# Optimization experiments

Hardware: AMD Instinct MI355X
Metric: run time of the kernel (lower is better)

Reference implementation:

```python
import jax, jax.numpy as jnp
import numpy as np

N, C, H, W = 16, 256, 128, 128
TC = max(8, C // 32)  # temp_c
EPS = 1e-5


def setup_inputs() -> dict:
    key = jax.random.key(0)
    ks = jax.random.split(key, 10)
    x = jax.random.normal(ks[0], (N, C, H, W), jnp.float32)
    # conv1: 1x1, C -> TC (weight squeezed to [TC, C])
    w1 = jax.random.normal(ks[1], (TC, C), jnp.float32) * 0.05
    b1 = jnp.zeros((TC,), jnp.float32)
    # BatchNorm2d (inference form)
    bn_gamma = jnp.ones((TC,), jnp.float32)
    bn_beta = jnp.zeros((TC,), jnp.float32)
    bn_mean = jnp.zeros((TC,), jnp.float32)
    bn_var = jnp.ones((TC,), jnp.float32)
    # conv2: kernel (1,2), TC -> C, squeezed to [C, TC, 2]
    w2 = jax.random.normal(ks[2], (C, TC, 2), jnp.float32) * 0.1
    b2 = jnp.zeros((C,), jnp.float32)
    # conv3: kernel (2,1), TC -> C, squeezed to [C, TC, 2]
    w3 = jax.random.normal(ks[3], (C, TC, 2), jnp.float32) * 0.1
    b3 = jnp.zeros((C,), jnp.float32)
    # conv4: kernel (1,2), TC -> C, squeezed to [C, TC, 2]
    w4 = jax.random.normal(ks[4], (C, TC, 2), jnp.float32) * 0.1
    b4 = jnp.zeros((C,), jnp.float32)
    return dict(x=x, w1=w1, b1=b1, bn_gamma=bn_gamma, bn_beta=bn_beta,
                bn_mean=bn_mean, bn_var=bn_var, w2=w2, b2=b2, w3=w3, b3=b3,
                w4=w4, b4=b4)


def reference(x, w1, b1, bn_gamma, bn_beta, bn_mean, bn_var,
              w2, b2, w3, b3, w4, b4):
    n, c, Hh, Ww = x.shape
    # avg/max pools along W (per-row), H (per-col), and global (per-channel)
    cat_h = jnp.stack([x.mean(3), x.max(3)], axis=-1)            # [n,c,H,2]
    cat_w = jnp.stack([x.mean(2), x.max(2)], axis=-1)            # [n,c,W,2]
    cat_c = jnp.stack([x.mean((2, 3)), x.max((2, 3))], -1)[:, :, None, :]  # [n,c,1,2]
    x_cat = jnp.concatenate([cat_h, cat_w, cat_c], axis=2)       # [n,c,H+W+1,2]
    # 1x1 conv + BN (inference) + h_swish
    y = jnp.einsum('ncsk,tc->ntsk', x_cat, w1) + b1[None, :, None, None]
    inv = bn_gamma / jnp.sqrt(bn_var + EPS)
    y = (y - bn_mean[None, :, None, None]) * inv[None, :, None, None] \
        + bn_beta[None, :, None, None]
    y = y * jnp.clip(y + 3.0, 0.0, 6.0) / 6.0                    # h_swish
    # split
    xh = y[:, :, :Hh, :]               # [n,tc,H,2]
    xw = y[:, :, Hh:Hh + Ww, :]        # [n,tc,W,2]
    xc = y[:, :, Hh + Ww, :]           # [n,tc,2]
    # tiny convs (kernels collapse to contractions over (tc, k)) + sigmoid
    a_h = jax.nn.sigmoid(jnp.einsum('nthk,otk->noh', xh, w2) + b2[None, :, None])  # [n,C,H]
    a_w = jax.nn.sigmoid(jnp.einsum('ntwk,otk->now', xw, w3) + b3[None, :, None])  # [n,C,W]
    a_c = jax.nn.sigmoid(jnp.einsum('ntk,otk->no', xc, w4) + b4[None, :])          # [n,C]
    return x * a_w[:, :, None, :] * a_h[:, :, :, None] * a_c[:, :, None, None]
```

## Files before the change

kernel.cpp:

```cpp
#include <hip/hip_runtime.h>
#include <math.h>

#define N_ 16
#define C_ 256
#define H_ 128
#define W_ 128
#define TC_ 8
#define S_ 257
#define EPS_ 1e-5f
#define NBLK 512
#define BPN 32
#define PPB 8

#define XCT_OFF  0
#define AH_OFF   2105344
#define AW_OFF   (AH_OFF + 524288)
#define Y256_OFF (AW_OFF + 524288)

typedef float f4n __attribute__((ext_vector_type(4)));

__global__ __launch_bounds__(256, 2) void k1_stats(
    const float* __restrict__ x, float* __restrict__ xcat)
{
    const int b = blockIdx.x;
    const int tid = threadIdx.x;
    __shared__ __align__(16) float smf[9472];

    float2 (*rowp)[33] = reinterpret_cast<float2(*)[33]>(smf);
    float4* scr_s = reinterpret_cast<float4*>(smf + 8448);
    float4* scr_m = reinterpret_cast<float4*>(smf + 8960);
    const int rg = tid >> 5;

    for (int u = 0; u < PPB; ++u) {
        const int p = b * PPB + u;
        const float4* xt = reinterpret_cast<const float4*>(x) + (size_t)p * 4096;
        float2* xcat2 = reinterpret_cast<float2*>(xcat) + (size_t)p * S_;

        float4 cs = make_float4(0.f, 0.f, 0.f, 0.f);
        float4 cm = make_float4(-INFINITY, -INFINITY, -INFINITY, -INFINITY);

        #pragma unroll
        for (int k = 0; k < 16; ++k) {
            const float4 v = xt[k * 256 + tid];
            cs.x += v.x; cs.y += v.y; cs.z += v.z; cs.w += v.w;
            cm.x = fmaxf(cm.x, v.x); cm.y = fmaxf(cm.y, v.y);
            cm.z = fmaxf(cm.z, v.z); cm.w = fmaxf(cm.w, v.w);
            const float rs = (v.x + v.y) + (v.z + v.w);
            const float rm = fmaxf(fmaxf(v.x, v.y), fmaxf(v.z, v.w));
            rowp[k * 8 + rg][tid & 31] = make_float2(rs, rm);
        }

        cs.x += __shfl_xor(cs.x, 32); cs.y += __shfl_xor(cs.y, 32);
        cs.z += __shfl_xor(cs.z, 32); cs.w += __shfl_xor(cs.w, 32);
        cm.x = fmaxf(cm.x, __shfl_xor(cm.x, 32));
        cm.y = fmaxf(cm.y, __shfl_xor(cm.y, 32));
        cm.z = fmaxf(cm.z, __shfl_xor(cm.z, 32));
        cm.w = fmaxf(cm.w, __shfl_xor(cm.w, 32));

        const int wv = tid >> 6, ln = tid & 63;
        if (ln < 32) { scr_s[wv * 32 + ln] = cs; scr_m[wv * 32 + ln] = cm; }
        __syncthreads();

        if (tid >= 128) {
            const int h = tid - 128;
            float2 q0 = rowp[h][0];
            float s = q0.x, m = q0.y;
            #pragma unroll
            for (int j = 1; j < 32; ++j) {
                const float2 q = rowp[h][j];
                s += q.x; m = fmaxf(m, q.y);
            }
            xcat2[h] = make_float2(s * (1.f / 128.f), m);
        }

        if (tid < 32) {
            const float4 s0 = scr_s[tid],      s1 = scr_s[32 + tid],
                         s2 = scr_s[64 + tid], s3 = scr_s[96 + tid];
            const float4 m0 = scr_m[tid],      m1 = scr_m[32 + tid],
                         m2 = scr_m[64 + tid], m3 = scr_m[96 + tid];
            float4 S, M;
            S.x = (s0.x + s1.x) + (s2.x + s3.x);
            S.y = (s0.y + s1.y) + (s2.y + s3.y);
            S.z = (s0.z + s1.z) + (s2.z + s3.z);
            S.w = (s0.w + s1.w) + (s2.w + s3.w);
            M.x = fmaxf(fmaxf(m0.x, m1.x), fmaxf(m2.x, m3.x));
            M.y = fmaxf(fmaxf(m0.y, m1.y), fmaxf(m2.y, m3.y));
            M.z = fmaxf(fmaxf(m0.z, m1.z), fmaxf(m2.z, m3.z));
            M.w = fmaxf(fmaxf(m0.w, m1.w), fmaxf(m2.w, m3.w));

            const int w0 = 4 * tid;
            xcat2[128 + w0 + 0] = make_float2(S.x * (1.f / 128.f), M.x);
            xcat2[128 + w0 + 1] = make_float2(S.y * (1.f / 128.f), M.y);
            xcat2[128 + w0 + 2] = make_float2(S.z * (1.f / 128.f), M.z);
            xcat2[128 + w0 + 3] = make_float2(S.w * (1.f / 128.f), M.w);

            float gs = (S.x + S.y) + (S.z + S.w);
            float gm = fmaxf(fmaxf(M.x, M.y), fmaxf(M.z, M.w));
            #pragma unroll
            for (int m = 16; m >= 1; m >>= 1) {
                gs += __shfl_xor(gs, m);
                gm = fmaxf(gm, __shfl_xor(gm, m));
            }
            if (tid == 0) xcat2[256] = make_float2(gs * (1.f / 16384.f), gm);
        }
        __syncthreads();
    }
}

__global__ __launch_bounds__(256, 2) void k2_attn(
    const float* __restrict__ xcat,
    const float* __restrict__ w1, const float* __restrict__ b1,
    const float* __restrict__ gam, const float* __restrict__ bet,
    const float* __restrict__ mu, const float* __restrict__ var,
    const float* __restrict__ w2, const float* __restrict__ b2,
    const float* __restrict__ w3, const float* __restrict__ b3,
    float* __restrict__ ahg, float* __restrict__ awg, float* __restrict__ y256g)
{
    const int b = blockIdx.x;
    const int n = b >> 5, cg = b & 31;
    const int tid = threadIdx.x;
    __shared__ __align__(16) float smf[6448];

    float* w1s = smf;
    float* red = smf + 2048;
    float* ys  = smf + 6272;
    const float2* xc2 = reinterpret_cast<const float2*>(xcat) + (size_t)n * C_ * S_;
    const int s0 = cg * 8;

    for (int i = tid; i < TC_ * C_; i += 256) w1s[i] = w1[i];
    __syncthreads();

    {
        const int cgrp = tid >> 3, si = tid & 7;
        const int s = s0 + si;
        float acc[16];
        #pragma unroll
        for (int j = 0; j < 16; ++j) acc[j] = 0.f;
        #pragma unroll
        for (int i = 0; i < 8; ++i) {
            const int c = cgrp * 8 + i;
            const float2 v = xc2[c * S_ + s];
            #pragma unroll
            for (int t = 0; t < TC_; ++t) {
                const float w = w1s[t * C_ + c];
                acc[t * 2 + 0] += v.x * w;
                acc[t * 2 + 1] += v.y * w;
            }
        }
        #pragma unroll
        for (int j = 0; j < 16; ++j) red[(si * 16 + j) * 33 + cgrp] = acc[j];
    }
    __syncthreads();

    if (tid < 128) {
        const int si2 = tid >> 4, j = tid & 15, t = j >> 1;
        float z = 0.f;
        #pragma unroll
        for (int g = 0; g < 32; ++g) z += red[(si2 * 16 + j) * 33 + g];
        const float inv = gam[t] * rsqrtf(var[t] + EPS_);
        float y = (z + b1[t] - mu[t]) * inv + bet[t];
        y = y * fminf(fmaxf(y + 3.f, 0.f), 6.f) * (1.f / 6.f);
        ys[si2 * 17 + j] = y;
    }
    __syncthreads();

    if (cg == BPN - 1) {
        const int c = tid;
        const float2 v = xc2[c * S_ + 256];
        float pj[16];
        #pragma unroll
        for (int t = 0; t < TC_; ++t) {
            const float w = w1s[t * C_ + c];
            pj[t * 2 + 0] = v.x * w;
            pj[t * 2 + 1] = v.y * w;
        }
        __syncthreads();
        float* red2 = smf;
        float* redB = smf + 4400;
        #pragma unroll
        for (int j = 0; j < 16; ++j) red2[tid * 17 + j] = pj[j];
        __syncthreads();
        {
            const int g = tid >> 4, j = tid & 15;
            float z = 0.f;
            #pragma unroll
            for (int m = 0; m < 16; ++m) z += red2[(g * 16 + m) * 17 + j];
            redB[j * 17 + g] = z;
        }
        __syncthreads();
        if (tid < 16) {
            const int j = tid, t = j >> 1;
            float z = 0.f;
            #pragma unroll
            for (int g = 0; g < 16; ++g) z += redB[j * 17 + g];
            const float inv = gam[t] * rsqrtf(var[t] + EPS_);
            float y = (z + b1[t] - mu[t]) * inv + bet[t];
            y = y * fminf(fmaxf(y + 3.f, 0.f), 6.f) * (1.f / 6.f);
            y256g[n * 16 + j] = y;
        }
        __syncthreads();
    }

    {
        const int o = tid;
        const bool is_h = (cg < 16);
        const float* wX = is_h ? w2 : w3;
        const float zb = is_h ? b2[o] : b3[o];
        float4 wr[4];
        const float4* wv = reinterpret_cast<const float4*>(wX + o * 16);
        #pragma unroll
        for (int q = 0; q < 4; ++q) wr[q] = wv[q];

        float r[8];
        #pragma unroll
        for (int si = 0; si < 8; ++si) {
            float z = zb;
            #pragma unroll
            for (int q = 0; q < 4; ++q) {
                z += ys[si * 17 + q * 4 + 0] * wr[q].x
                   + ys[si * 17 + q * 4 + 1] * wr[q].y
                   + ys[si * 17 + q * 4 + 2] * wr[q].z
                   + ys[si * 17 + q * 4 + 3] * wr[q].w;
            }
            r[si] = 1.f / (1.f + expf(-z));
        }
        float* og = is_h ? (ahg + (size_t)(n * C_ + o) * H_ + s0)
                         : (awg + (size_t)(n * C_ + o) * W_ + (s0 - 128));
        *reinterpret_cast<float4*>(og)     = make_float4(r[0], r[1], r[2], r[3]);
        *reinterpret_cast<float4*>(og + 4) = make_float4(r[4], r[5], r[6], r[7]);
    }
}

__global__ __launch_bounds__(256, 2) void k3_apply(
    const float* __restrict__ x,
    const float* __restrict__ w4, const float* __restrict__ b4,
    const float* __restrict__ ahg, const float* __restrict__ awg,
    const float* __restrict__ y256g, float* __restrict__ out)
{
    const int b = blockIdx.x;
    const int n = b >> 5, cg = b & 31, c0 = cg * 8;
    const int tid = threadIdx.x;
    __shared__ __align__(16) float smf[2064];

    float* acs = smf;
    float* ahl = smf + 16;
    float* awl = smf + 1040;

    if (tid < 8) {
        const int o = c0 + tid;
        float z = b4[o];
        #pragma unroll
        for (int j = 0; j < 16; ++j) z += y256g[n * 16 + j] * w4[o * 16 + j];
        acs[tid] = 1.f / (1.f + expf(-z));
    }
    __syncthreads();

    for (int idx = tid; idx < 8 * 128; idx += 256) {
        const int u = idx >> 7, h = idx & 127, o = c0 + u;
        ahl[idx] = acs[u] * ahg[(size_t)(n * C_ + o) * H_ + h];
        awl[idx] = awg[(size_t)(n * C_ + o) * W_ + h];
    }
    __syncthreads();

    const float4* awv = reinterpret_cast<const float4*>(awl);
    for (int u = 0; u < PPB; ++u) {
        const int p = b * PPB + u;
        const f4n* x4 = reinterpret_cast<const f4n*>(x) + (size_t)p * 4096;
        f4n* o4 = reinterpret_cast<f4n*>(out) + (size_t)p * 4096;

        const float4 a = awv[u * 32 + (tid & 31)];
        #pragma unroll
        for (int k = 0; k < 16; ++k) {
            const int i4 = k * 256 + tid;
            f4n v = x4[i4];
            const float s = ahl[u * 128 + k * 8 + (tid >> 5)];
            v.x *= s * a.x; v.y *= s * a.y; v.z *= s * a.z; v.w *= s * a.w;
            __builtin_nontemporal_store(v, &o4[i4]);
        }
    }
}

extern "C" void kernel_launch(void* const* d_in, const int* in_sizes, int n_in,
                              void* d_out, int out_size, void* d_ws, size_t ws_size,
                              hipStream_t stream) {
    const float* x   = (const float*)d_in[0];
    const float* w1  = (const float*)d_in[1];
    const float* b1  = (const float*)d_in[2];
    const float* gam = (const float*)d_in[3];
    const float* bet = (const float*)d_in[4];
    const float* mu  = (const float*)d_in[5];
    const float* var = (const float*)d_in[6];
    const float* w2  = (const float*)d_in[7];
    const float* b2  = (const float*)d_in[8];
    const float* w3  = (const float*)d_in[9];
    const float* b3  = (const float*)d_in[10];
    const float* w4  = (const float*)d_in[11];
    const float* b4  = (const float*)d_in[12];

    float* ws    = (float*)d_ws;
    float* xcat  = ws + XCT_OFF;
    float* ahg   = ws + AH_OFF;
    float* awg   = ws + AW_OFF;
    float* y256g = ws + Y256_OFF;
    float* out   = (float*)d_out;

    k1_stats<<<NBLK, 256, 0, stream>>>(x, xcat);
    k2_attn<<<NBLK, 256, 0, stream>>>(xcat, w1, b1, gam, bet, mu, var,
                                      w2, b2, w3, b3, ahg, awg, y256g);
    k3_apply<<<NBLK, 256, 0, stream>>>(x, w4, b4, ahg, awg, y256g, out);
}
```

Baseline: 177.4 us.

## Map one wavefront per plane in stats kernel with DPP row reductions

The stats kernel now gives each 64-lane wavefront a whole 128x128 plane instead of having a 256-thread block loop over eight planes. Row sums and maxes are reduced with DPP row shifts inside registers rather than through shared memory. This removes the LDS staging and both block barriers, and the grid grows to 1024 blocks with a higher occupancy hint. In exchange, each wave does 64 sequential loads plus DPP reduction chains per iteration, and the per-row results are written to global memory by single lanes as scattered small stores.

```diff
diff --git a/kernel.cpp b/kernel.cpp
--- a/kernel.cpp
+++ b/kernel.cpp
@@ -19,92 +19,88 @@
 
 typedef float f4n __attribute__((ext_vector_type(4)));
 
-__global__ __launch_bounds__(256, 2) void k1_stats(
+template <int CTRL>
+__device__ __forceinline__ float dpp_zf(float x) {
+    return __int_as_float(__builtin_amdgcn_update_dpp(
+        0, __float_as_int(x), CTRL, 0xF, 0xF, true));
+}
+template <int CTRL>
+__device__ __forceinline__ float dpp_keep(float x) {
+    return __int_as_float(__builtin_amdgcn_update_dpp(
+        __float_as_int(x), __float_as_int(x), CTRL, 0xF, 0xF, false));
+}
+#define SHR1 0x111
+#define SHR2 0x112
+#define SHR4 0x114
+#define SHR8 0x118
+#define BC15 0x142
+
+__device__ __forceinline__ float rowsum32(float x) {
+    x += dpp_zf<SHR1>(x);
+    x += dpp_zf<SHR2>(x);
+    x += dpp_zf<SHR4>(x);
+    x += dpp_zf<SHR8>(x);
+    x += dpp_zf<BC15>(x);
+    return x;
+}
+__device__ __forceinline__ float rowmax32(float x) {
+    x = fmaxf(x, dpp_keep<SHR1>(x));
+    x = fmaxf(x, dpp_keep<SHR2>(x));
+    x = fmaxf(x, dpp_keep<SHR4>(x));
+    x = fmaxf(x, dpp_keep<SHR8>(x));
+    x = fmaxf(x, dpp_keep<BC15>(x));
+    return x;
+}
+
+__global__ __launch_bounds__(256, 4) void k1_stats(
     const float* __restrict__ x, float* __restrict__ xcat)
 {
-    const int b = blockIdx.x;
-    const int tid = threadIdx.x;
-    __shared__ __align__(16) float smf[9472];
-
-    float2 (*rowp)[33] = reinterpret_cast<float2(*)[33]>(smf);
-    float4* scr_s = reinterpret_cast<float4*>(smf + 8448);
-    float4* scr_m = reinterpret_cast<float4*>(smf + 8960);
-    const int rg = tid >> 5;
-
-    for (int u = 0; u < PPB; ++u) {
-        const int p = b * PPB + u;
-        const float4* xt = reinterpret_cast<const float4*>(x) + (size_t)p * 4096;
-        float2* xcat2 = reinterpret_cast<float2*>(xcat) + (size_t)p * S_;
-
-        float4 cs = make_float4(0.f, 0.f, 0.f, 0.f);
-        float4 cm = make_float4(-INFINITY, -INFINITY, -INFINITY, -INFINITY);
-
-        #pragma unroll
-        for (int k = 0; k < 16; ++k) {
-            const float4 v = xt[k * 256 + tid];
-            cs.x += v.x; cs.y += v.y; cs.z += v.z; cs.w += v.w;
-            cm.x = fmaxf(cm.x, v.x); cm.y = fmaxf(cm.y, v.y);
-            cm.z = fmaxf(cm.z, v.z); cm.w = fmaxf(cm.w, v.w);
-            const float rs = (v.x + v.y) + (v.z + v.w);
-            const float rm = fmaxf(fmaxf(v.x, v.y), fmaxf(v.z, v.w));
-            rowp[k * 8 + rg][tid & 31] = make_float2(rs, rm);
-        }
-
-        cs.x += __shfl_xor(cs.x, 32); cs.y += __shfl_xor(cs.y, 32);
-        cs.z += __shfl_xor(cs.z, 32); cs.w += __shfl_xor(cs.w, 32);
-        cm.x = fmaxf(cm.x, __shfl_xor(cm.x, 32));
-        cm.y = fmaxf(cm.y, __shfl_xor(cm.y, 32));
-        cm.z = fmaxf(cm.z, __shfl_xor(cm.z, 32));
-        cm.w = fmaxf(cm.w, __shfl_xor(cm.w, 32));
-
-        const int wv = tid >> 6, ln = tid & 63;
-        if (ln < 32) { scr_s[wv * 32 + ln] = cs; scr_m[wv * 32 + ln] = cm; }
-        __syncthreads();
-
-        if (tid >= 128) {
-            const int h = tid - 128;
-            float2 q0 = rowp[h][0];
-            float s = q0.x, m = q0.y;
-            #pragma unroll
-            for (int j = 1; j < 32; ++j) {
-                const float2 q = rowp[h][j];
-                s += q.x; m = fmaxf(m, q.y);
-            }
-            xcat2[h] = make_float2(s * (1.f / 128.f), m);
-        }
-
-        if (tid < 32) {
-            const float4 s0 = scr_s[tid],      s1 = scr_s[32 + tid],
-                         s2 = scr_s[64 + tid], s3 = scr_s[96 + tid];
-            const float4 m0 = scr_m[tid],      m1 = scr_m[32 + tid],
-                         m2 = scr_m[64 + tid], m3 = scr_m[96 + tid];
-            float4 S, M;
-            S.x = (s0.x + s1.x) + (s2.x + s3.x);
-            S.y = (s0.y + s1.y) + (s2.y + s3.y);
-            S.z = (s0.z + s1.z) + (s2.z + s3.z);
-            S.w = (s0.w + s1.w) + (s2.w + s3.w);
-            M.x = fmaxf(fmaxf(m0.x, m1.x), fmaxf(m2.x, m3.x));
-            M.y = fmaxf(fmaxf(m0.y, m1.y), fmaxf(m2.y, m3.y));
-            M.z = fmaxf(fmaxf(m0.z, m1.z), fmaxf(m2.z, m3.z));
-            M.w = fmaxf(fmaxf(m0.w, m1.w), fmaxf(m2.w, m3.w));
-
-            const int w0 = 4 * tid;
-            xcat2[128 + w0 + 0] = make_float2(S.x * (1.f / 128.f), M.x);
-            xcat2[128 + w0 + 1] = make_float2(S.y * (1.f / 128.f), M.y);
-            xcat2[128 + w0 + 2] = make_float2(S.z * (1.f / 128.f), M.z);
-            xcat2[128 + w0 + 3] = make_float2(S.w * (1.f / 128.f), M.w);
-
-            float gs = (S.x + S.y) + (S.z + S.w);
-            float gm = fmaxf(fmaxf(M.x, M.y), fmaxf(M.z, M.w));
-            #pragma unroll
-            for (int m = 16; m >= 1; m >>= 1) {
-                gs += __shfl_xor(gs, m);
-                gm = fmaxf(gm, __shfl_xor(gm, m));
-            }
-            if (tid == 0) xcat2[256] = make_float2(gs * (1.f / 16384.f), gm);
-        }
-        __syncthreads();
-    }
+    const int tid = threadIdx.x, lane = tid & 63, wv = tid >> 6;
+    const int p = blockIdx.x * 4 + wv;
+    const float4* xt = reinterpret_cast<const float4*>(x) + (size_t)p * 4096;
+    float2* xcat2 = reinterpret_cast<float2*>(xcat) + (size_t)p * S_;
+
+    float4 cs = make_float4(0.f, 0.f, 0.f, 0.f);
+    float4 cm = make_float4(-INFINITY, -INFINITY, -INFINITY, -INFINITY);
+
+    #pragma unroll 8
+    for (int it = 0; it < 64; ++it) {
+        const float4 v = xt[it * 64 + lane];
+        cs.x += v.x; cs.y += v.y; cs.z += v.z; cs.w += v.w;
+        cm.x = fmaxf(cm.x, v.x); cm.y = fmaxf(cm.y, v.y);
+        cm.z = fmaxf(cm.z, v.z); cm.w = fmaxf(cm.w, v.w);
+
+        float rs = (v.x + v.y) + (v.z + v.w);
+        float rm = fmaxf(fmaxf(v.x, v.y), fmaxf(v.z, v.w));
+        rs = rowsum32(rs);
+        rm = rowmax32(rm);
+        if ((lane & 31) == 31)
+            xcat2[it * 2 + (lane >> 5)] = make_float2(rs * (1.f / 128.f), rm);
+    }
+
+    cs.x += __shfl_xor(cs.x, 32); cs.y += __shfl_xor(cs.y, 32);
+    cs.z += __shfl_xor(cs.z, 32); cs.w += __shfl_xor(cs.w, 32);
+    cm.x = fmaxf(cm.x, __shfl_xor(cm.x, 32));
+    cm.y = fmaxf(cm.y, __shfl_xor(cm.y, 32));
+    cm.z = fmaxf(cm.z, __shfl_xor(cm.z, 32));
+    cm.w = fmaxf(cm.w, __shfl_xor(cm.w, 32));
+
+    if (lane < 32) {
+        const int w0 = 4 * lane;
+        xcat2[128 + w0 + 0] = make_float2(cs.x * (1.f / 128.f), cm.x);
+        xcat2[128 + w0 + 1] = make_float2(cs.y * (1.f / 128.f), cm.y);
+        xcat2[128 + w0 + 2] = make_float2(cs.z * (1.f / 128.f), cm.z);
+        xcat2[128 + w0 + 3] = make_float2(cs.w * (1.f / 128.f), cm.w);
+    }
+
+    float gs = (cs.x + cs.y) + (cs.z + cs.w);
+    float gm = fmaxf(fmaxf(cm.x, cm.y), fmaxf(cm.z, cm.w));
+    #pragma unroll
+    for (int m = 16; m >= 1; m >>= 1) {
+        gs += __shfl_xor(gs, m);
+        gm = fmaxf(gm, __shfl_xor(gm, m));
+    }
+    if (lane == 0) xcat2[256] = make_float2(gs * (1.f / 16384.f), gm);
 }
 
 __global__ __launch_bounds__(256, 2) void k2_attn(
@@ -304,7 +300,7 @@
     float* y256g = ws + Y256_OFF;
     float* out   = (float*)d_out;
 
-    k1_stats<<<NBLK, 256, 0, stream>>>(x, xcat);
+    k1_stats<<<1024, 256, 0, stream>>>(x, xcat);
     k2_attn<<<NBLK, 256, 0, stream>>>(xcat, w1, b1, gam, bet, mu, var,
                                       w2, b2, w3, b3, ahg, awg, y256g);
     k3_apply<<<NBLK, 256, 0, stream>>>(x, w4, b4, ahg, awg, y256g, out);
```

Result: faster. 173.8 us (-2.0%).
